# Kernel optimization log

Measured on AMD Instinct MI355X. Metric: run time of the kernel, lower is better.

## Reference

```python
import jax, jax.numpy as jnp
import numpy as np

B, T, V, D = 128, 128, 64, 32
Q, E, PLM = 5, 8, 768
D_STATIC, N_CLASS = 16, 2
ALPHA = 0.5


def _glorot(key, shape):
    lim = (6.0 / (shape[-2] + shape[-1])) ** 0.5
    return jax.random.uniform(key, shape, jnp.float32, -lim, lim)


def setup_inputs() -> dict:
    key = jax.random.key(0)
    ks = jax.random.split(key, 30)
    data = jax.random.normal(ks[0], (B, T, V), jnp.float32)
    mask = (jax.random.uniform(ks[1], (B, T, V)) < 0.3).astype(jnp.float32)
    P = jnp.concatenate([data, mask], axis=-1)  # [b, t, 2v]
    return {
        "P": P,
        "P_static": jax.random.normal(ks[2], (B, D_STATIC), jnp.float32),
        "P_avg_interval": jax.random.uniform(ks[3], (B, T, V)) * 10.0,
        "P_length": jax.random.randint(ks[4], (B, 1), T // 2, T + 1),
        "P_time": jax.random.uniform(ks[5], (B, T)),
        "P_var_plm_rep_tensor": jax.random.normal(ks[6], (V, PLM), jnp.float32),
        # Value_Encoder: Linear(1, D) + ReLU
        "w_val": _glorot(ks[7], (1, D))[0], "b_val": jnp.zeros((D,), jnp.float32),
        # Time_Encoder: periodic Linear(1, D-1), linear Linear(1, 1)
        "w_per": _glorot(ks[8], (1, D - 1))[0], "b_per": jnp.zeros((D - 1,), jnp.float32),
        "w_lin": _glorot(ks[9], (1, 1))[0], "b_lin": jnp.zeros((1,), jnp.float32),
        "emb1": jax.random.normal(ks[10], (V, D), jnp.float32),
        # prior_to_state MLP: PLM -> 2D -> Q
        "Ws1": _glorot(ks[11], (PLM, 2 * D)), "bs1": jnp.zeros((2 * D,), jnp.float32),
        "Ws2": _glorot(ks[12], (2 * D, Q)), "bs2": jnp.zeros((Q,), jnp.float32),
        # prior_to_graph MLP: PLM -> 2D -> E
        "Wg1": _glorot(ks[13], (PLM, 2 * D)), "bg1": jnp.zeros((2 * D,), jnp.float32),
        "Wg2": _glorot(ks[14], (2 * D, E)), "bg2": jnp.zeros((E,), jnp.float32),
        "rarity_W": jax.random.normal(ks[15], (V, V), jnp.float32),
        # hypernet gate params (nodes_num == Q): W [Q, 2D+1, D], b [Q, D]
        "Wu": _glorot(ks[16], (Q, 2 * D + 1, D)), "bu": _glorot(ks[17], (Q, D)),
        "Wr": _glorot(ks[18], (Q, 2 * D + 1, D)), "br": _glorot(ks[19], (Q, D)),
        "Wcand": _glorot(ks[20], (Q, 2 * D + 1, D)), "bcand": _glorot(ks[21], (Q, D)),
        # static embedding + classifier
        "W_se": _glorot(ks[22], (D_STATIC, V)), "b_se": jnp.zeros((V,), jnp.float32),
        "Wc1": _glorot(ks[23], (2 * V, 200)), "bc1": jnp.zeros((200,), jnp.float32),
        "Wc2": _glorot(ks[24], (200, N_CLASS)), "bc2": jnp.zeros((N_CLASS,), jnp.float32),
    }


def _forward(P, P_static, P_avg_interval, P_length, P_time, P_var_plm_rep_tensor,
             w_val, b_val, w_per, b_per, w_lin, b_lin, emb1,
             Ws1, bs1, Ws2, bs2, Wg1, bg1, Wg2, bg2, rarity_W,
             Wu, bu, Wr, br, Wcand, bcand, W_se, b_se, Wc1, bc1, Wc2, bc2):
    b, t, v2 = P.shape
    v = v2 // 2
    d = emb1.shape[1]
    data, mask = P[:, :, :v], P[:, :, v:]            # [b,t,v] each
    mk = mask[..., None]
    # embeddings: value + absolute time + node embedding, all masked
    value_emb = jax.nn.relu(data[..., None] * w_val + b_val) * mk          # [b,t,v,d]
    tt = P_time[:, :, None, None]                                          # [b,t,1,1]
    time_emb = jnp.concatenate([tt * w_lin + b_lin,
                                jnp.sin(tt * w_per + b_per)], -1) * mk     # [b,t,v,d]
    obs_emb = (value_emb + time_emb + emb1[None, None]) * mk               # [b,t,v,d]

    # PLM-prior hypernet vectors (identical across batch -> computed once, broadcast)
    var_vector = jax.nn.relu(P_var_plm_rep_tensor @ Ws1 + bs1) @ Ws2 + bs2  # [v,Q]
    gvec = jax.nn.relu(P_var_plm_rep_tensor @ Wg1 + bg1) @ Wg2 + bg2        # [v,E]
    gvec = gvec / jnp.maximum(jnp.linalg.norm(gvec, axis=-1, keepdims=True), 1e-12)
    adj = jax.nn.softmax(gvec @ gvec.T, axis=-1)                            # [v,v]

    var_total_obs = mask.sum(axis=1)                                        # [b,v]
    eye = jnp.eye(v, dtype=P.dtype)
    lengths = P_length[:, 0].astype(jnp.int32)                              # [b]

    def gate(inp, W, bb):
        # hypernet-generated per-node GRU gate: einsum('nd,dio->nio') + bmm, fused
        return (jnp.einsum('bvi,vq,qio->bvo', inp, var_vector, W)
                + jnp.einsum('vq,qo->vo', var_vector, bb))

    def step(carry, xs):
        h, out = carry
        cur_obs, m, cur_avg, s = xs
        rarity = ALPHA * jnp.tanh(cur_avg / (var_total_obs + 1.0))          # [b,v]
        rsm = -rarity_W * jnp.abs(rarity[:, :, None] - rarity[:, None, :])  # [b,v,v]
        amask = m[:, :, None] * m[:, None, :]   # rows of unobserved zeroed, observed cols = 1
        cur_adj = adj * (1.0 + rsm) * amask * (1.0 - eye) + eye             # [b,v,v]
        x = jnp.concatenate([cur_obs, rarity[..., None]], -1)               # [b,v,d+1]
        comb = jnp.einsum('bij,bjk->bik', cur_adj, jnp.concatenate([x, h], -1))
        r = jax.nn.sigmoid(gate(comb, Wr, br))
        u = jax.nn.sigmoid(gate(comb, Wu, bu))
        h_r = r * h  # original mutates h[nodes_ind] = r*h[nodes_ind] before candidate
        cand = jnp.tanh(gate(jnp.concatenate([x, h_r], -1), Wcand, bcand))
        h_new = (1.0 - u) * h_r + u * cand
        h = jnp.where((m > 0.5)[..., None], h_new, h)  # scatter only observed nodes
        out = jnp.where((s == lengths - 1)[:, None, None], h, out)
        return (h, out), None

    xs = (jnp.moveaxis(obs_emb, 1, 0), jnp.moveaxis(mask, 1, 0),
          jnp.moveaxis(P_avg_interval, 1, 0), jnp.arange(t, dtype=jnp.int32))
    h0 = jnp.zeros((b, v, d), P.dtype)
    (_, output), _ = jax.lax.scan(step, (h0, jnp.zeros_like(h0)), xs)

    static_emb = P_static @ W_se + b_se                                     # [b,v]
    feat = jnp.concatenate([output.sum(-1), static_emb], -1)                # [b,2v]
    return jax.nn.relu(feat @ Wc1 + bc1) @ Wc2 + bc2                        # [b,n_class]


def reference(P, P_static, P_avg_interval, P_length, P_time, P_var_plm_rep_tensor,
              w_val, b_val, w_per, b_per, w_lin, b_lin, emb1,
              Ws1, bs1, Ws2, bs2, Wg1, bg1, Wg2, bg2, rarity_W,
              Wu, bu, Wr, br, Wcand, bcand, W_se, b_se, Wc1, bc1, Wc2, bc2):
    return _forward(P, P_static, P_avg_interval, P_length, P_time, P_var_plm_rep_tensor,
                    w_val, b_val, w_per, b_per, w_lin, b_lin, emb1,
                    Ws1, bs1, Ws2, bs2, Wg1, bg1, Wg2, bg2, rarity_W,
                    Wu, bu, Wr, br, Wcand, bcand, W_se, b_se, Wc1, bc1, Wc2, bc2)
```

## Files before the change

kernel.cpp:

```cpp
#include <hip/hip_runtime.h>
#include <hip/hip_bf16.h>
#include <math.h>

#define BB 128
#define TT 128
#define VV 64
#define DD 32
#define NQ 5

typedef short bf16x8 __attribute__((ext_vector_type(8)));
typedef float f32x4 __attribute__((ext_vector_type(4)));

#define MFMA(a,b,c) __builtin_amdgcn_mfma_f32_16x16x32_bf16(a,b,c,0,0,0)
#define SB_DS() __builtin_amdgcn_sched_barrier(0x7F)

__device__ __forceinline__ float sigm(float x){ return 1.0f/(1.0f+__expf(-x)); }
__device__ __forceinline__ float tanhfast(float x){ return 2.0f/(1.0f+__expf(-2.0f*x)) - 1.0f; }
__device__ __forceinline__ unsigned short f2bf(float x){
  unsigned u = __float_as_uint(x);
  u += 0x7FFFu + ((u>>16)&1u);
  return (unsigned short)(u>>16);
}
__device__ __forceinline__ float bf2f(unsigned short h){
  return __uint_as_float(((unsigned)h)<<16);
}

union bfu { bf16x8 v; unsigned u[4]; unsigned short s[8]; };

__device__ __forceinline__ void split8(const float* x, bfu& H, bfu& L){
  #pragma unroll
  for (int i = 0; i < 4; ++i){
    const float a = x[2*i], c = x[2*i+1];
    const __hip_bfloat162 hp = __float22bfloat162_rn(make_float2(a, c));
    unsigned hu; __builtin_memcpy(&hu, &hp, 4);
    H.u[i] = hu;
    const float ah = __uint_as_float(hu << 16);
    const float ch = __uint_as_float(hu & 0xFFFF0000u);
    const __hip_bfloat162 lp = __float22bfloat162_rn(make_float2(a - ah, c - ch));
    unsigned lu; __builtin_memcpy(&lu, &lp, 4);
    L.u[i] = lu;
  }
}


__global__ __launch_bounds__(64)
void k_mlp(const float* __restrict__ Pplm,
           const float* __restrict__ Ws1, const float* __restrict__ bs1,
           const float* __restrict__ Ws2, const float* __restrict__ bs2,
           const float* __restrict__ Wg1, const float* __restrict__ bg1,
           const float* __restrict__ Wg2, const float* __restrict__ bg2,
           float* __restrict__ vv_ws, float* __restrict__ gn_ws)
{
  __shared__ float sH[64], sG[64], sgv[8];
  const int v = blockIdx.x, j = threadIdx.x;
  float a = bs1[j], g = bg1[j];
  for (int k = 0; k < 768; ++k){
    const float p = Pplm[v*768 + k];
    a = fmaf(p, Ws1[k*64 + j], a);
    g = fmaf(p, Wg1[k*64 + j], g);
  }
  sH[j] = fmaxf(a, 0.f);
  sG[j] = fmaxf(g, 0.f);
  __syncthreads();
  if (j < 5){
    float acc = bs2[j];
    for (int k = 0; k < 64; ++k) acc = fmaf(sH[k], Ws2[k*5 + j], acc);
    vv_ws[v*5 + j] = acc;
  }
  if (j < 8){
    float acc = bg2[j];
    for (int k = 0; k < 64; ++k) acc = fmaf(sG[k], Wg2[k*8 + j], acc);
    sgv[j] = acc;
  }
  __syncthreads();
  if (j == 0){
    float n = 0.f;
    for (int e = 0; e < 8; ++e) n += sgv[e]*sgv[e];
    n = fmaxf(sqrtf(n), 1e-12f);
    for (int e = 0; e < 8; ++e) gn_ws[v*8 + e] = sgv[e]/n;
  }
}

__global__ __launch_bounds__(64)
void k_adj(const float* __restrict__ gn_ws, float* __restrict__ adj_ws)
{
  const int v = blockIdx.x, j = threadIdx.x;
  float sc = 0.f;
  #pragma unroll
  for (int e = 0; e < 8; ++e) sc += gn_ws[v*8+e]*gn_ws[j*8+e];
  float mx = sc;
  for (int off = 32; off > 0; off >>= 1) mx = fmaxf(mx, __shfl_xor(mx, off));
  const float ex = __expf(sc - mx);
  float sm = ex;
  for (int off = 32; off > 0; off >>= 1) sm += __shfl_xor(sm, off);
  adj_ws[v*64 + j] = ex / sm;
}

__global__ __launch_bounds__(256)
void k_vto(const float* __restrict__ P, float* __restrict__ vto_ws)
{
  const int idx = blockIdx.x*256 + threadIdx.x;
  if (idx >= BB*VV) return;
  const int b = idx/VV, v = idx%VV;
  float s = 0.f;
  for (int t = 0; t < TT; ++t) s += P[((size_t)(b*TT+t))*128 + 64 + v];
  vto_ws[idx] = s;
}

__global__ __launch_bounds__(256)
void k_bpack(const float* __restrict__ Wr, const float* __restrict__ br,
             const float* __restrict__ Wu, const float* __restrict__ bu,
             const float* __restrict__ Wc, const float* __restrict__ bc,
             unsigned short* __restrict__ Bru, unsigned short* __restrict__ Bcn,
             float* __restrict__ sideRU, float* __restrict__ sideC)
{
  const int idx = blockIdx.x*256 + threadIdx.x;
  if (idx < 20480){
    const int f = idx >> 9, rem = idx & 511, l = rem >> 3, j = rem & 7;
    const int p = f & 1, kt = (f>>1)&1, e = f>>2;
    const int kp = kt*32 + (l>>4)*8 + j;
    const int k = (kp < 32) ? kp : kp + 1;
    const int o = p*16 + (l&15);
    const int q = (e < 5) ? e : e - 5;
    const float* W = (e < 5) ? Wr : Wu;
    Bru[idx] = f2bf(W[(q*65 + k)*32 + o]);
  } else if (idx < 30720){
    const int i2 = idx - 20480;
    const int f = i2 >> 9, rem = i2 & 511, l = rem >> 3, j = rem & 7;
    const int p = f & 1, kt = (f>>1)&1, e = f>>2;
    const int kp = kt*32 + (l>>4)*8 + j;
    const int k = (kp < 32) ? kp : kp + 1;
    const int o = p*16 + (l&15);
    Bcn[i2] = f2bf(Wc[(e*65 + k)*32 + o]);
  } else if (idx < 31360){
    const int i3 = idx - 30720;
    const int e = i3 >> 6, rem = i3 & 63, o = rem >> 1, s = rem & 1;
    const int q = (e < 5) ? e : e - 5;
    float v;
    if (s == 0) v = (e < 5) ? Wr[(q*65 + 32)*32 + o] : Wu[(q*65 + 32)*32 + o];
    else        v = (e < 5) ? br[q*32 + o] : bu[q*32 + o];
    sideRU[i3] = v;
  } else if (idx < 31680){
    const int i4 = idx - 31360;
    const int e = i4 >> 6, rem = i4 & 63, o = rem >> 1, s = rem & 1;
    sideC[i4] = s ? bc[e*32 + o] : Wc[(e*65 + 32)*32 + o];
  }
}


__global__ __launch_bounds__(256, 1)
void tedgn_main(const float* __restrict__ P, const float* __restrict__ Pstatic,
                const float* __restrict__ Pavg, const int* __restrict__ Plen,
                const float* __restrict__ Ptime,
                const float* __restrict__ w_val, const float* __restrict__ b_val,
                const float* __restrict__ w_per, const float* __restrict__ b_per,
                const float* __restrict__ w_lin, const float* __restrict__ b_lin,
                const float* __restrict__ emb1, const float* __restrict__ rarW,
                const float* __restrict__ Wse, const float* __restrict__ bse,
                const float* __restrict__ Wc1, const float* __restrict__ bc1,
                const float* __restrict__ Wc2, const float* __restrict__ bc2,
                const float* __restrict__ vv_ws, const float* __restrict__ adjb_ws,
                const float* __restrict__ vto_ws,
                const unsigned short* __restrict__ Bru_ws,
                const unsigned short* __restrict__ Bc_ws,
                const float* __restrict__ sideRU_ws, const float* __restrict__ sideC_ws,
                float* __restrict__ out)
{
  __shared__ __align__(16) unsigned short B0T[2][2][64][72];
  __shared__ __align__(16) unsigned short s_Wru[20480];
  __shared__ __align__(16) unsigned short s_Wc[10240];
  __shared__ __align__(16) float A1f[4][16][68];
  __shared__ __align__(16) float hrF[4][16][36];
  __shared__ __align__(16) float s_rar[2][64];
  __shared__ __align__(16) float s_m[2][64];
  __shared__ float s_sru[640], s_scd[320];
  __shared__ float s_outf[64][33];
  __shared__ float s_feat[128], s_hid[200];

  const int tid  = threadIdx.x;
  const int lane = tid & 63;
  const int wid  = tid >> 6;
  const int l15  = lane & 15;
  const int l16g = lane >> 4;
  const int kgo  = l16g * 8;
  const int R    = wid * 16;
  const int v_own = R + l15;
  const int b    = blockIdx.x;
  const int len  = Plen[b];

  for (int i = tid; i < 640; i += 256) s_sru[i] = sideRU_ws[i];
  for (int i = tid; i < 320; i += 256) s_scd[i] = sideC_ws[i];
  {
    const uint4* src1 = (const uint4*)Bru_ws;
    uint4* dst1 = (uint4*)s_Wru;
    for (int i = tid; i < 2560; i += 256) dst1[i] = src1[i];
    const uint4* src2 = (const uint4*)Bc_ws;
    uint4* dst2 = (uint4*)s_Wc;
    for (int i = tid; i < 1280; i += 256) dst2[i] = src2[i];
  }

  float adjb_r[2][8], rarW_r[2][8];
  #pragma unroll
  for (int kt = 0; kt < 2; ++kt)
    #pragma unroll
    for (int j = 0; j < 8; ++j){
      adjb_r[kt][j] = adjb_ws[v_own*64 + kt*32 + kgo + j];
      rarW_r[kt][j] = rarW   [v_own*64 + kt*32 + kgo + j];
    }
  float embr[8], wvr[8], bvr[8], wpr[8], bpr[8];
  #pragma unroll
  for (int j = 0; j < 8; ++j){
    const int d = kgo + j;
    embr[j] = emb1[v_own*DD + d];
    wvr[j]  = w_val[d];
    bvr[j]  = b_val[d];
    wpr[j]  = (d == 0) ? w_lin[0] : w_per[d-1];
    bpr[j]  = (d == 0) ? b_lin[0] : b_per[d-1];
  }
  float vvr[4][NQ];
  #pragma unroll
  for (int j = 0; j < 4; ++j)
    #pragma unroll
    for (int q = 0; q < NQ; ++q)
      vvr[j][q] = vv_ws[(R + l16g*4 + j)*NQ + q];
  const float vto_own = vto_ws[b*VV + v_own];

  float h[2][4]    = {{0.f,0.f,0.f,0.f},{0.f,0.f,0.f,0.f}};
  float outr[2][4] = {{0.f,0.f,0.f,0.f},{0.f,0.f,0.f,0.f}};
  bfu xfH, xfL;
  float rar_own, m_own;

  {
    const float pd = P[(size_t)(b*TT)*128 + v_own];
    const float pm = P[(size_t)(b*TT)*128 + 64 + v_own];
    const float pa = Pavg[(size_t)(b*TT)*VV + v_own];
    const float pt = Ptime[b*TT];
    const float rar_n = 0.5f * tanhfast(pa / (vto_own + 1.f));
    float xv[8];
    #pragma unroll
    for (int j = 0; j < 8; ++j){
      const int d = kgo + j;
      const float tearg = fmaf(pt, wpr[j], bpr[j]);
      const float te = (d == 0) ? tearg : __sinf(tearg);
      const float ve = fmaxf(fmaf(pd, wvr[j], bvr[j]), 0.f);
      xv[j] = (ve + te + embr[j]) * pm;
    }
    split8(xv, xfH, xfL);
    #pragma unroll
    for (int j = 0; j < 8; ++j){
      B0T[0][0][kgo + j][v_own] = xfH.s[j];
      B0T[0][1][kgo + j][v_own] = xfL.s[j];
    }
    *(uint2*)&B0T[0][0][32 + l15][R + l16g*4] = make_uint2(0u, 0u);
    *(uint2*)&B0T[0][1][32 + l15][R + l16g*4] = make_uint2(0u, 0u);
    *(uint2*)&B0T[0][0][48 + l15][R + l16g*4] = make_uint2(0u, 0u);
    *(uint2*)&B0T[0][1][48 + l15][R + l16g*4] = make_uint2(0u, 0u);
    if (l16g == 0){
      s_rar[0][v_own] = rar_n;
      s_m[0][v_own]   = pm;
    }
    rar_own = rar_n;
    m_own   = pm;
  }
  __syncthreads();

  #pragma clang loop unroll(disable)
  for (int t = 0; t < TT; ++t){
    const int cur = t & 1, nxt = cur ^ 1;

    float pd = 0.f, pm = 0.f, pa = 0.f, pt = 0.f;
    const bool more = (t + 1 < TT);
    if (more){
      pd = P[(size_t)(b*TT + t + 1)*128 + v_own];
      pm = P[(size_t)(b*TT + t + 1)*128 + 64 + v_own];
      pa = Pavg[(size_t)(b*TT + t + 1)*VV + v_own];
      pt = Ptime[b*TT + t + 1];
    }

    bfu aAh[2], aAl[2];
    float crar = 0.f;
    #pragma unroll
    for (int kt = 0; kt < 2; ++kt){
      const float4 r0 = *(const float4*)&s_rar[cur][kt*32 + kgo];
      const float4 r1 = *(const float4*)&s_rar[cur][kt*32 + kgo + 4];
      const float4 m0 = *(const float4*)&s_m[cur][kt*32 + kgo];
      const float4 m1 = *(const float4*)&s_m[cur][kt*32 + kgo + 4];
      const float rj[8] = {r0.x,r0.y,r0.z,r0.w,r1.x,r1.y,r1.z,r1.w};
      const float mj[8] = {m0.x,m0.y,m0.z,m0.w,m1.x,m1.y,m1.z,m1.w};
      float av[8];
      #pragma unroll
      for (int j = 0; j < 8; ++j){
        const int k = kt*32 + kgo + j;
        const float e1 = fmaf(-rarW_r[kt][j], fabsf(rar_own - rj[j]), 1.0f);
        const float a  = adjb_r[kt][j] * e1 * (m_own * mj[j]);
        av[j] = (k == v_own) ? 1.0f : a;
        crar = fmaf(av[j], rj[j], crar);
      }
      split8(av, aAh[kt], aAl[kt]);
    }
    crar += __shfl_xor(crar, 16);
    crar += __shfl_xor(crar, 32);
    if (l16g == 0) A1f[wid][l15][64] = crar;

    #pragma unroll
    for (int n = 0; n < 4; ++n){
      f32x4 acc = {0.f,0.f,0.f,0.f};
      #pragma unroll
      for (int kt = 0; kt < 2; ++kt){
        const bf16x8 bh = *(const bf16x8*)&B0T[cur][0][n*16 + l15][kt*32 + kgo];
        const bf16x8 bl = *(const bf16x8*)&B0T[cur][1][n*16 + l15][kt*32 + kgo];
        acc = MFMA(aAh[kt].v, bh, acc);
        acc = MFMA(aAl[kt].v, bh, acc);
        acc = MFMA(aAh[kt].v, bl, acc);
      }
      const int col = n*16 + l15;
      #pragma unroll
      for (int j = 0; j < 4; ++j) A1f[wid][l16g*4 + j][col] = acc[j];
    }
    SB_DS();

    bfu aH[2], aL[2];
    #pragma unroll
    for (int kt = 0; kt < 2; ++kt){
      float xv[8];
      *(float4*)&xv[0] = *(const float4*)&A1f[wid][l15][kt*32 + kgo];
      *(float4*)&xv[4] = *(const float4*)&A1f[wid][l15][kt*32 + kgo + 4];
      split8(xv, aH[kt], aL[kt]);
    }
    float a64f[4];
    #pragma unroll
    for (int j = 0; j < 4; ++j) a64f[j] = A1f[wid][l16g*4 + j][64];

    float hr[2][4], uu[2][4];
    {
      f32x4 ag[10][2];
      #pragma unroll
      for (int e = 0; e < 10; ++e)
        #pragma unroll
        for (int p2 = 0; p2 < 2; ++p2){
          const float2 wb = *(const float2*)&s_sru[e*64 + (p2*16 + l15)*2];
          #pragma unroll
          for (int j = 0; j < 4; ++j) ag[e][p2][j] = fmaf(a64f[j], wb.x, wb.y);
        }
      #pragma unroll
      for (int e = 0; e < 10; ++e)
        #pragma unroll
        for (int p2 = 0; p2 < 2; ++p2){
          const bf16x8 w0 = *(const bf16x8*)&s_Wru[(((e*2+0)*2+p2)*64 + lane)*8];
          const bf16x8 w1 = *(const bf16x8*)&s_Wru[(((e*2+1)*2+p2)*64 + lane)*8];
          ag[e][p2] = MFMA(aH[0].v, w0, ag[e][p2]);
          ag[e][p2] = MFMA(aL[0].v, w0, ag[e][p2]);
          ag[e][p2] = MFMA(aH[1].v, w1, ag[e][p2]);
          ag[e][p2] = MFMA(aL[1].v, w1, ag[e][p2]);
        }
      #pragma unroll
      for (int p2 = 0; p2 < 2; ++p2)
        #pragma unroll
        for (int j = 0; j < 4; ++j){
          const float pr = vvr[j][0]*ag[0][p2][j] + vvr[j][1]*ag[1][p2][j]
                         + vvr[j][2]*ag[2][p2][j] + vvr[j][3]*ag[3][p2][j]
                         + vvr[j][4]*ag[4][p2][j];
          hr[p2][j] = sigm(pr) * h[p2][j];
          hrF[wid][l16g*4 + j][p2*16 + l15] = hr[p2][j];
        }
      #pragma unroll
      for (int p2 = 0; p2 < 2; ++p2)
        #pragma unroll
        for (int j = 0; j < 4; ++j){
          const float pu = vvr[j][0]*ag[5][p2][j] + vvr[j][1]*ag[6][p2][j]
                         + vvr[j][2]*ag[7][p2][j] + vvr[j][3]*ag[8][p2][j]
                         + vvr[j][4]*ag[9][p2][j];
          uu[p2][j] = sigm(pu);
        }
    }
    SB_DS();

    {
      bfu hH, hL;
      {
        float hv[8];
        *(float4*)&hv[0] = *(const float4*)&hrF[wid][l15][kgo];
        *(float4*)&hv[4] = *(const float4*)&hrF[wid][l15][kgo + 4];
        split8(hv, hH, hL);
      }
      float rar_cj[4], m_cj[4];
      #pragma unroll
      for (int j = 0; j < 4; ++j){
        rar_cj[j] = s_rar[cur][R + l16g*4 + j];
        m_cj[j]   = s_m[cur][R + l16g*4 + j];
      }
      f32x4 ag[5][2];
      #pragma unroll
      for (int e = 0; e < 5; ++e)
        #pragma unroll
        for (int p2 = 0; p2 < 2; ++p2){
          const float2 wb = *(const float2*)&s_scd[e*64 + (p2*16 + l15)*2];
          #pragma unroll
          for (int j = 0; j < 4; ++j) ag[e][p2][j] = fmaf(rar_cj[j], wb.x, wb.y);
        }
      #pragma unroll
      for (int e = 0; e < 5; ++e)
        #pragma unroll
        for (int p2 = 0; p2 < 2; ++p2){
          const bf16x8 w0 = *(const bf16x8*)&s_Wc[(((e*2+0)*2+p2)*64 + lane)*8];
          const bf16x8 w1 = *(const bf16x8*)&s_Wc[(((e*2+1)*2+p2)*64 + lane)*8];
          ag[e][p2] = MFMA(xfH.v, w0, ag[e][p2]);
          ag[e][p2] = MFMA(xfL.v, w0, ag[e][p2]);
          ag[e][p2] = MFMA(hH.v,  w1, ag[e][p2]);
          ag[e][p2] = MFMA(hL.v,  w1, ag[e][p2]);
        }
      const bool snap = (t == len - 1);
      #pragma unroll
      for (int p2 = 0; p2 < 2; ++p2)
        #pragma unroll
        for (int j = 0; j < 4; ++j){
          const float pc = vvr[j][0]*ag[0][p2][j] + vvr[j][1]*ag[1][p2][j]
                         + vvr[j][2]*ag[2][p2][j] + vvr[j][3]*ag[3][p2][j]
                         + vvr[j][4]*ag[4][p2][j];
          const float cd = tanhfast(pc);
          const float hn = fmaf(uu[p2][j], cd - hr[p2][j], hr[p2][j]);
          const float hf = (m_cj[j] > 0.5f) ? hn : h[p2][j];
          h[p2][j] = hf;
          if (snap) outr[p2][j] = hf;
        }
    }

    {
      float h8[8] = {h[0][0],h[0][1],h[0][2],h[0][3],h[1][0],h[1][1],h[1][2],h[1][3]};
      bfu HH, HL;
      split8(h8, HH, HL);
      *(uint2*)&B0T[nxt][0][32 + l15][R + l16g*4] = make_uint2(HH.u[0], HH.u[1]);
      *(uint2*)&B0T[nxt][1][32 + l15][R + l16g*4] = make_uint2(HL.u[0], HL.u[1]);
      *(uint2*)&B0T[nxt][0][48 + l15][R + l16g*4] = make_uint2(HH.u[2], HH.u[3]);
      *(uint2*)&B0T[nxt][1][48 + l15][R + l16g*4] = make_uint2(HL.u[2], HL.u[3]);
    }

    if (more){
      const float rar_n = 0.5f * tanhfast(pa / (vto_own + 1.f));
      float xv[8];
      #pragma unroll
      for (int j = 0; j < 8; ++j){
        const int d = kgo + j;
        const float tearg = fmaf(pt, wpr[j], bpr[j]);
        const float te = (d == 0) ? tearg : __sinf(tearg);
        const float ve = fmaxf(fmaf(pd, wvr[j], bvr[j]), 0.f);
        xv[j] = (ve + te + embr[j]) * pm;
      }
      split8(xv, xfH, xfL);
      #pragma unroll
      for (int j = 0; j < 8; ++j){
        B0T[nxt][0][kgo + j][v_own] = xfH.s[j];
        B0T[nxt][1][kgo + j][v_own] = xfL.s[j];
      }
      if (l16g == 0){
        s_rar[nxt][v_own] = rar_n;
        s_m[nxt][v_own]   = pm;
      }
      rar_own = rar_n;
      m_own   = pm;
    }
    __syncthreads();
  }

  #pragma unroll
  for (int p2 = 0; p2 < 2; ++p2)
    #pragma unroll
    for (int j = 0; j < 4; ++j)
      s_outf[R + l16g*4 + j][p2*16 + l15] = outr[p2][j];
  __syncthreads();
  if (tid < VV){
    float s = 0.f;
    #pragma unroll
    for (int d = 0; d < DD; ++d) s += s_outf[tid][d];
    s_feat[tid] = s;
  } else if (tid < 2*VV){
    const int v = tid - VV;
    float se = bse[v];
    #pragma unroll
    for (int k = 0; k < 16; ++k) se = fmaf(Pstatic[b*16 + k], Wse[k*VV + v], se);
    s_feat[VV + v] = se;
  }
  __syncthreads();
  if (tid < 200){
    float a = bc1[tid];
    for (int k = 0; k < 128; ++k) a = fmaf(s_feat[k], Wc1[k*200 + tid], a);
    s_hid[tid] = fmaxf(a, 0.f);
  }
  __syncthreads();
  if (tid < 2){
    float a = bc2[tid];
    for (int k = 0; k < 200; ++k) a = fmaf(s_hid[k], Wc2[k*2 + tid], a);
    out[b*2 + tid] = a;
  }
}


extern "C" void kernel_launch(void* const* d_in, const int* in_sizes, int n_in,
                              void* d_out, int out_size, void* d_ws, size_t ws_size,
                              hipStream_t stream) {
  (void)in_sizes; (void)n_in; (void)out_size; (void)ws_size;
  const float* P       = (const float*)d_in[0];
  const float* Pstatic = (const float*)d_in[1];
  const float* Pavg    = (const float*)d_in[2];
  const int*   Plen    = (const int*)  d_in[3];
  const float* Ptime   = (const float*)d_in[4];
  const float* Pplm    = (const float*)d_in[5];
  const float* w_val   = (const float*)d_in[6];
  const float* b_val   = (const float*)d_in[7];
  const float* w_per   = (const float*)d_in[8];
  const float* b_per   = (const float*)d_in[9];
  const float* w_lin   = (const float*)d_in[10];
  const float* b_lin   = (const float*)d_in[11];
  const float* emb1    = (const float*)d_in[12];
  const float* Ws1     = (const float*)d_in[13];
  const float* bs1     = (const float*)d_in[14];
  const float* Ws2     = (const float*)d_in[15];
  const float* bs2     = (const float*)d_in[16];
  const float* Wg1     = (const float*)d_in[17];
  const float* bg1     = (const float*)d_in[18];
  const float* Wg2     = (const float*)d_in[19];
  const float* bg2     = (const float*)d_in[20];
  const float* rarW    = (const float*)d_in[21];
  const float* Wu      = (const float*)d_in[22];
  const float* bu      = (const float*)d_in[23];
  const float* Wr      = (const float*)d_in[24];
  const float* br      = (const float*)d_in[25];
  const float* Wcand   = (const float*)d_in[26];
  const float* bcand   = (const float*)d_in[27];
  const float* Wse     = (const float*)d_in[28];
  const float* bse     = (const float*)d_in[29];
  const float* Wc1     = (const float*)d_in[30];
  const float* bc1     = (const float*)d_in[31];
  const float* Wc2     = (const float*)d_in[32];
  const float* bc2     = (const float*)d_in[33];

  float* ws = (float*)d_ws;
  float*          vv_ws   = ws;
  float*          gn_ws   = ws + 320;
  float*          adjb_ws = ws + 832;
  float*          vto_ws  = ws + 4928;
  unsigned short* Bru_ws  = (unsigned short*)(ws + 13120);
  unsigned short* Bc_ws   = (unsigned short*)(ws + 23360);
  float*          sideRU_ws = ws + 28480;
  float*          sideC_ws  = ws + 29120;

  k_mlp  <<<64, 64, 0, stream>>>(Pplm, Ws1, bs1, Ws2, bs2, Wg1, bg1, Wg2, bg2, vv_ws, gn_ws);
  k_adj  <<<64, 64, 0, stream>>>(gn_ws, adjb_ws);
  k_vto  <<<(BB*VV + 255)/256, 256, 0, stream>>>(P, vto_ws);
  k_bpack<<<124, 256, 0, stream>>>(Wr, br, Wu, bu, Wcand, bcand, Bru_ws, Bc_ws, sideRU_ws, sideC_ws);

  tedgn_main<<<BB, 256, 0, stream>>>(P, Pstatic, Pavg, Plen, Ptime,
                                     w_val, b_val, w_per, b_per, w_lin, b_lin,
                                     emb1, rarW, Wse, bse, Wc1, bc1, Wc2, bc2,
                                     vv_ws, adjb_ws, vto_ws,
                                     Bru_ws, Bc_ws, sideRU_ws, sideC_ws,
                                     (float*)d_out);
}
```

Measured before the change: 623.4 us.

## Split each row-block across two waves by output half, doubling block to 512 threads

The main recurrent kernel now launches 512 threads per batch element. Each pair of waves shares a 16-row block and splits the 32 hidden output columns between them, so each wave does half the MFMA work for the gate and candidate products. The aim is to shorten the serial per-timestep critical path by spreading the work over more waves per CU. In exchange it replaces the wave-local sched barriers with two extra block-wide __syncthreads per timestep, and the adjacency/rarity computation is duplicated in both waves of each pair.

```diff
diff --git a/kernel.cpp b/kernel.cpp
--- a/kernel.cpp
+++ b/kernel.cpp
@@ -12,7 +12,6 @@
 typedef float f32x4 __attribute__((ext_vector_type(4)));
 
 #define MFMA(a,b,c) __builtin_amdgcn_mfma_f32_16x16x32_bf16(a,b,c,0,0,0)
-#define SB_DS() __builtin_amdgcn_sched_barrier(0x7F)
 
 __device__ __forceinline__ float sigm(float x){ return 1.0f/(1.0f+__expf(-x)); }
 __device__ __forceinline__ float tanhfast(float x){ return 2.0f/(1.0f+__expf(-2.0f*x)) - 1.0f; }
@@ -39,6 +38,21 @@
     const __hip_bfloat162 lp = __float22bfloat162_rn(make_float2(a - ah, c - ch));
     unsigned lu; __builtin_memcpy(&lu, &lp, 4);
     L.u[i] = lu;
+  }
+}
+
+__device__ __forceinline__ void split4(const float* x, unsigned* H, unsigned* L){
+  #pragma unroll
+  for (int i = 0; i < 2; ++i){
+    const float a = x[2*i], c = x[2*i+1];
+    const __hip_bfloat162 hp = __float22bfloat162_rn(make_float2(a, c));
+    unsigned hu; __builtin_memcpy(&hu, &hp, 4);
+    H[i] = hu;
+    const float ah = __uint_as_float(hu << 16);
+    const float ch = __uint_as_float(hu & 0xFFFF0000u);
+    const __hip_bfloat162 lp = __float22bfloat162_rn(make_float2(a - ah, c - ch));
+    unsigned lu; __builtin_memcpy(&lu, &lp, 4);
+    L[i] = lu;
   }
 }
 
@@ -148,7 +162,7 @@
 }
 
 
-__global__ __launch_bounds__(256, 1)
+__global__ __launch_bounds__(512, 1)
 void tedgn_main(const float* __restrict__ P, const float* __restrict__ Pstatic,
                 const float* __restrict__ Pavg, const int* __restrict__ Plen,
                 const float* __restrict__ Ptime,
@@ -180,23 +194,26 @@
   const int tid  = threadIdx.x;
   const int lane = tid & 63;
   const int wid  = tid >> 6;
+  const int mq   = wid >> 1;
+  const int ph   = wid & 1;
   const int l15  = lane & 15;
   const int l16g = lane >> 4;
   const int kgo  = l16g * 8;
-  const int R    = wid * 16;
+  const int R    = mq * 16;
   const int v_own = R + l15;
+  const int oo   = ph*16 + l15;
   const int b    = blockIdx.x;
   const int len  = Plen[b];
 
-  for (int i = tid; i < 640; i += 256) s_sru[i] = sideRU_ws[i];
-  for (int i = tid; i < 320; i += 256) s_scd[i] = sideC_ws[i];
+  for (int i = tid; i < 640; i += 512) s_sru[i] = sideRU_ws[i];
+  for (int i = tid; i < 320; i += 512) s_scd[i] = sideC_ws[i];
   {
     const uint4* src1 = (const uint4*)Bru_ws;
     uint4* dst1 = (uint4*)s_Wru;
-    for (int i = tid; i < 2560; i += 256) dst1[i] = src1[i];
+    for (int i = tid; i < 2560; i += 512) dst1[i] = src1[i];
     const uint4* src2 = (const uint4*)Bc_ws;
     uint4* dst2 = (uint4*)s_Wc;
-    for (int i = tid; i < 1280; i += 256) dst2[i] = src2[i];
+    for (int i = tid; i < 1280; i += 512) dst2[i] = src2[i];
   }
 
   float adjb_r[2][8], rarW_r[2][8];
@@ -225,8 +242,8 @@
       vvr[j][q] = vv_ws[(R + l16g*4 + j)*NQ + q];
   const float vto_own = vto_ws[b*VV + v_own];
 
-  float h[2][4]    = {{0.f,0.f,0.f,0.f},{0.f,0.f,0.f,0.f}};
-  float outr[2][4] = {{0.f,0.f,0.f,0.f},{0.f,0.f,0.f,0.f}};
+  float h[4]    = {0.f,0.f,0.f,0.f};
+  float outr[4] = {0.f,0.f,0.f,0.f};
   bfu xfH, xfL;
   float rar_own, m_own;
 
@@ -246,18 +263,21 @@
       xv[j] = (ve + te + embr[j]) * pm;
     }
     split8(xv, xfH, xfL);
-    #pragma unroll
-    for (int j = 0; j < 8; ++j){
-      B0T[0][0][kgo + j][v_own] = xfH.s[j];
-      B0T[0][1][kgo + j][v_own] = xfL.s[j];
-    }
-    *(uint2*)&B0T[0][0][32 + l15][R + l16g*4] = make_uint2(0u, 0u);
-    *(uint2*)&B0T[0][1][32 + l15][R + l16g*4] = make_uint2(0u, 0u);
-    *(uint2*)&B0T[0][0][48 + l15][R + l16g*4] = make_uint2(0u, 0u);
-    *(uint2*)&B0T[0][1][48 + l15][R + l16g*4] = make_uint2(0u, 0u);
-    if (l16g == 0){
-      s_rar[0][v_own] = rar_n;
-      s_m[0][v_own]   = pm;
+    if (ph == 0){
+      #pragma unroll
+      for (int j = 0; j < 8; ++j){
+        B0T[0][0][kgo + j][v_own] = xfH.s[j];
+        B0T[0][1][kgo + j][v_own] = xfL.s[j];
+      }
+      *(uint2*)&B0T[0][0][32 + l15][R + l16g*4] = make_uint2(0u, 0u);
+      *(uint2*)&B0T[0][1][32 + l15][R + l16g*4] = make_uint2(0u, 0u);
+      if (l16g == 0){
+        s_rar[0][v_own] = rar_n;
+        s_m[0][v_own]   = pm;
+      }
+    } else {
+      *(uint2*)&B0T[0][0][48 + l15][R + l16g*4] = make_uint2(0u, 0u);
+      *(uint2*)&B0T[0][1][48 + l15][R + l16g*4] = make_uint2(0u, 0u);
     }
     rar_own = rar_n;
     m_own   = pm;
@@ -277,110 +297,105 @@
       pt = Ptime[b*TT + t + 1];
     }
 
-    bfu aAh[2], aAl[2];
-    float crar = 0.f;
-    #pragma unroll
-    for (int kt = 0; kt < 2; ++kt){
-      const float4 r0 = *(const float4*)&s_rar[cur][kt*32 + kgo];
-      const float4 r1 = *(const float4*)&s_rar[cur][kt*32 + kgo + 4];
-      const float4 m0 = *(const float4*)&s_m[cur][kt*32 + kgo];
-      const float4 m1 = *(const float4*)&s_m[cur][kt*32 + kgo + 4];
-      const float rj[8] = {r0.x,r0.y,r0.z,r0.w,r1.x,r1.y,r1.z,r1.w};
-      const float mj[8] = {m0.x,m0.y,m0.z,m0.w,m1.x,m1.y,m1.z,m1.w};
-      float av[8];
-      #pragma unroll
-      for (int j = 0; j < 8; ++j){
-        const int k = kt*32 + kgo + j;
-        const float e1 = fmaf(-rarW_r[kt][j], fabsf(rar_own - rj[j]), 1.0f);
-        const float a  = adjb_r[kt][j] * e1 * (m_own * mj[j]);
-        av[j] = (k == v_own) ? 1.0f : a;
-        crar = fmaf(av[j], rj[j], crar);
-      }
-      split8(av, aAh[kt], aAl[kt]);
-    }
-    crar += __shfl_xor(crar, 16);
-    crar += __shfl_xor(crar, 32);
-    if (l16g == 0) A1f[wid][l15][64] = crar;
-
-    #pragma unroll
-    for (int n = 0; n < 4; ++n){
-      f32x4 acc = {0.f,0.f,0.f,0.f};
+    {
+      bfu aAh[2], aAl[2];
+      float crar = 0.f;
       #pragma unroll
       for (int kt = 0; kt < 2; ++kt){
-        const bf16x8 bh = *(const bf16x8*)&B0T[cur][0][n*16 + l15][kt*32 + kgo];
-        const bf16x8 bl = *(const bf16x8*)&B0T[cur][1][n*16 + l15][kt*32 + kgo];
-        acc = MFMA(aAh[kt].v, bh, acc);
-        acc = MFMA(aAl[kt].v, bh, acc);
-        acc = MFMA(aAh[kt].v, bl, acc);
-      }
-      const int col = n*16 + l15;
-      #pragma unroll
-      for (int j = 0; j < 4; ++j) A1f[wid][l16g*4 + j][col] = acc[j];
-    }
-    SB_DS();
-
-    bfu aH[2], aL[2];
-    #pragma unroll
-    for (int kt = 0; kt < 2; ++kt){
-      float xv[8];
-      *(float4*)&xv[0] = *(const float4*)&A1f[wid][l15][kt*32 + kgo];
-      *(float4*)&xv[4] = *(const float4*)&A1f[wid][l15][kt*32 + kgo + 4];
-      split8(xv, aH[kt], aL[kt]);
-    }
-    float a64f[4];
-    #pragma unroll
-    for (int j = 0; j < 4; ++j) a64f[j] = A1f[wid][l16g*4 + j][64];
-
-    float hr[2][4], uu[2][4];
+        const float4 r0 = *(const float4*)&s_rar[cur][kt*32 + kgo];
+        const float4 r1 = *(const float4*)&s_rar[cur][kt*32 + kgo + 4];
+        const float4 m0 = *(const float4*)&s_m[cur][kt*32 + kgo];
+        const float4 m1 = *(const float4*)&s_m[cur][kt*32 + kgo + 4];
+        const float rj[8] = {r0.x,r0.y,r0.z,r0.w,r1.x,r1.y,r1.z,r1.w};
+        const float mj[8] = {m0.x,m0.y,m0.z,m0.w,m1.x,m1.y,m1.z,m1.w};
+        float av[8];
+        #pragma unroll
+        for (int j = 0; j < 8; ++j){
+          const int k = kt*32 + kgo + j;
+          const float e1 = fmaf(-rarW_r[kt][j], fabsf(rar_own - rj[j]), 1.0f);
+          const float a  = adjb_r[kt][j] * e1 * (m_own * mj[j]);
+          av[j] = (k == v_own) ? 1.0f : a;
+          crar = fmaf(av[j], rj[j], crar);
+        }
+        split8(av, aAh[kt], aAl[kt]);
+      }
+      crar += __shfl_xor(crar, 16);
+      crar += __shfl_xor(crar, 32);
+      if (ph == 0 && l16g == 0) A1f[mq][l15][64] = crar;
+
+      #pragma unroll
+      for (int ni = 0; ni < 2; ++ni){
+        const int n = 2*ph + ni;
+        f32x4 acc = {0.f,0.f,0.f,0.f};
+        #pragma unroll
+        for (int kt = 0; kt < 2; ++kt){
+          const bf16x8 bh = *(const bf16x8*)&B0T[cur][0][n*16 + l15][kt*32 + kgo];
+          const bf16x8 bl = *(const bf16x8*)&B0T[cur][1][n*16 + l15][kt*32 + kgo];
+          acc = MFMA(aAh[kt].v, bh, acc);
+          acc = MFMA(aAl[kt].v, bh, acc);
+          acc = MFMA(aAh[kt].v, bl, acc);
+        }
+        const int col = n*16 + l15;
+        #pragma unroll
+        for (int j = 0; j < 4; ++j) A1f[mq][l16g*4 + j][col] = acc[j];
+      }
+    }
+    __syncthreads();
+
+    float hr[4], uu[4];
     {
-      f32x4 ag[10][2];
-      #pragma unroll
-      for (int e = 0; e < 10; ++e)
+      bfu aH[2], aL[2];
+      #pragma unroll
+      for (int kt = 0; kt < 2; ++kt){
+        float xv[8];
+        *(float4*)&xv[0] = *(const float4*)&A1f[mq][l15][kt*32 + kgo];
+        *(float4*)&xv[4] = *(const float4*)&A1f[mq][l15][kt*32 + kgo + 4];
+        split8(xv, aH[kt], aL[kt]);
+      }
+      float a64f[4];
+      #pragma unroll
+      for (int j = 0; j < 4; ++j) a64f[j] = A1f[mq][l16g*4 + j][64];
+
+      f32x4 ag[10];
+      #pragma unroll
+      for (int e = 0; e < 10; ++e){
+        const float2 wb = *(const float2*)&s_sru[e*64 + oo*2];
         #pragma unroll
-        for (int p2 = 0; p2 < 2; ++p2){
-          const float2 wb = *(const float2*)&s_sru[e*64 + (p2*16 + l15)*2];
-          #pragma unroll
-          for (int j = 0; j < 4; ++j) ag[e][p2][j] = fmaf(a64f[j], wb.x, wb.y);
-        }
-      #pragma unroll
-      for (int e = 0; e < 10; ++e)
-        #pragma unroll
-        for (int p2 = 0; p2 < 2; ++p2){
-          const bf16x8 w0 = *(const bf16x8*)&s_Wru[(((e*2+0)*2+p2)*64 + lane)*8];
-          const bf16x8 w1 = *(const bf16x8*)&s_Wru[(((e*2+1)*2+p2)*64 + lane)*8];
-          ag[e][p2] = MFMA(aH[0].v, w0, ag[e][p2]);
-          ag[e][p2] = MFMA(aL[0].v, w0, ag[e][p2]);
-          ag[e][p2] = MFMA(aH[1].v, w1, ag[e][p2]);
-          ag[e][p2] = MFMA(aL[1].v, w1, ag[e][p2]);
-        }
-      #pragma unroll
-      for (int p2 = 0; p2 < 2; ++p2)
-        #pragma unroll
-        for (int j = 0; j < 4; ++j){
-          const float pr = vvr[j][0]*ag[0][p2][j] + vvr[j][1]*ag[1][p2][j]
-                         + vvr[j][2]*ag[2][p2][j] + vvr[j][3]*ag[3][p2][j]
-                         + vvr[j][4]*ag[4][p2][j];
-          hr[p2][j] = sigm(pr) * h[p2][j];
-          hrF[wid][l16g*4 + j][p2*16 + l15] = hr[p2][j];
-        }
-      #pragma unroll
-      for (int p2 = 0; p2 < 2; ++p2)
-        #pragma unroll
-        for (int j = 0; j < 4; ++j){
-          const float pu = vvr[j][0]*ag[5][p2][j] + vvr[j][1]*ag[6][p2][j]
-                         + vvr[j][2]*ag[7][p2][j] + vvr[j][3]*ag[8][p2][j]
-                         + vvr[j][4]*ag[9][p2][j];
-          uu[p2][j] = sigm(pu);
-        }
-    }
-    SB_DS();
+        for (int j = 0; j < 4; ++j) ag[e][j] = fmaf(a64f[j], wb.x, wb.y);
+      }
+      #pragma unroll
+      for (int e = 0; e < 10; ++e){
+        const bf16x8 w0 = *(const bf16x8*)&s_Wru[(((e*2+0)*2+ph)*64 + lane)*8];
+        const bf16x8 w1 = *(const bf16x8*)&s_Wru[(((e*2+1)*2+ph)*64 + lane)*8];
+        ag[e] = MFMA(aH[0].v, w0, ag[e]);
+        ag[e] = MFMA(aL[0].v, w0, ag[e]);
+        ag[e] = MFMA(aH[1].v, w1, ag[e]);
+        ag[e] = MFMA(aL[1].v, w1, ag[e]);
+      }
+      #pragma unroll
+      for (int j = 0; j < 4; ++j){
+        const float pr = vvr[j][0]*ag[0][j] + vvr[j][1]*ag[1][j]
+                       + vvr[j][2]*ag[2][j] + vvr[j][3]*ag[3][j]
+                       + vvr[j][4]*ag[4][j];
+        hr[j] = sigm(pr) * h[j];
+        hrF[mq][l16g*4 + j][oo] = hr[j];
+      }
+      #pragma unroll
+      for (int j = 0; j < 4; ++j){
+        const float pu = vvr[j][0]*ag[5][j] + vvr[j][1]*ag[6][j]
+                       + vvr[j][2]*ag[7][j] + vvr[j][3]*ag[8][j]
+                       + vvr[j][4]*ag[9][j];
+        uu[j] = sigm(pu);
+      }
+    }
+    __syncthreads();
 
     {
       bfu hH, hL;
       {
         float hv[8];
-        *(float4*)&hv[0] = *(const float4*)&hrF[wid][l15][kgo];
-        *(float4*)&hv[4] = *(const float4*)&hrF[wid][l15][kgo + 4];
+        *(float4*)&hv[0] = *(const float4*)&hrF[mq][l15][kgo];
+        *(float4*)&hv[4] = *(const float4*)&hrF[mq][l15][kgo + 4];
         split8(hv, hH, hL);
       }
       float rar_cj[4], m_cj[4];
@@ -389,84 +404,73 @@
         rar_cj[j] = s_rar[cur][R + l16g*4 + j];
         m_cj[j]   = s_m[cur][R + l16g*4 + j];
       }
-      f32x4 ag[5][2];
-      #pragma unroll
-      for (int e = 0; e < 5; ++e)
+      f32x4 ag[5];
+      #pragma unroll
+      for (int e = 0; e < 5; ++e){
+        const float2 wb = *(const float2*)&s_scd[e*64 + oo*2];
         #pragma unroll
-        for (int p2 = 0; p2 < 2; ++p2){
-          const float2 wb = *(const float2*)&s_scd[e*64 + (p2*16 + l15)*2];
+        for (int j = 0; j < 4; ++j) ag[e][j] = fmaf(rar_cj[j], wb.x, wb.y);
+      }
+      #pragma unroll
+      for (int e = 0; e < 5; ++e){
+        const bf16x8 w0 = *(const bf16x8*)&s_Wc[(((e*2+0)*2+ph)*64 + lane)*8];
+        const bf16x8 w1 = *(const bf16x8*)&s_Wc[(((e*2+1)*2+ph)*64 + lane)*8];
+        ag[e] = MFMA(xfH.v, w0, ag[e]);
+        ag[e] = MFMA(xfL.v, w0, ag[e]);
+        ag[e] = MFMA(hH.v,  w1, ag[e]);
+        ag[e] = MFMA(hL.v,  w1, ag[e]);
+      }
+      const bool snap = (t == len - 1);
+      #pragma unroll
+      for (int j = 0; j < 4; ++j){
+        const float pc = vvr[j][0]*ag[0][j] + vvr[j][1]*ag[1][j]
+                       + vvr[j][2]*ag[2][j] + vvr[j][3]*ag[3][j]
+                       + vvr[j][4]*ag[4][j];
+        const float cd = tanhfast(pc);
+        const float hn = fmaf(uu[j], cd - hr[j], hr[j]);
+        const float hf = (m_cj[j] > 0.5f) ? hn : h[j];
+        h[j] = hf;
+        if (snap) outr[j] = hf;
+      }
+      {
+        unsigned H2[2], L2[2];
+        split4(h, H2, L2);
+        *(uint2*)&B0T[nxt][0][32 + oo][R + l16g*4] = make_uint2(H2[0], H2[1]);
+        *(uint2*)&B0T[nxt][1][32 + oo][R + l16g*4] = make_uint2(L2[0], L2[1]);
+      }
+      if (more){
+        const float rar_n = 0.5f * tanhfast(pa / (vto_own + 1.f));
+        float xv[8];
+        #pragma unroll
+        for (int j = 0; j < 8; ++j){
+          const int d = kgo + j;
+          const float tearg = fmaf(pt, wpr[j], bpr[j]);
+          const float te = (d == 0) ? tearg : __sinf(tearg);
+          const float ve = fmaxf(fmaf(pd, wvr[j], bvr[j]), 0.f);
+          xv[j] = (ve + te + embr[j]) * pm;
+        }
+        split8(xv, xfH, xfL);
+        if (ph == 0){
           #pragma unroll
-          for (int j = 0; j < 4; ++j) ag[e][p2][j] = fmaf(rar_cj[j], wb.x, wb.y);
+          for (int j = 0; j < 8; ++j){
+            B0T[nxt][0][kgo + j][v_own] = xfH.s[j];
+            B0T[nxt][1][kgo + j][v_own] = xfL.s[j];
+          }
+          if (l16g == 0){
+            s_rar[nxt][v_own] = rar_n;
+            s_m[nxt][v_own]   = pm;
+          }
         }
-      #pragma unroll
-      for (int e = 0; e < 5; ++e)
-        #pragma unroll
-        for (int p2 = 0; p2 < 2; ++p2){
-          const bf16x8 w0 = *(const bf16x8*)&s_Wc[(((e*2+0)*2+p2)*64 + lane)*8];
-          const bf16x8 w1 = *(const bf16x8*)&s_Wc[(((e*2+1)*2+p2)*64 + lane)*8];
-          ag[e][p2] = MFMA(xfH.v, w0, ag[e][p2]);
-          ag[e][p2] = MFMA(xfL.v, w0, ag[e][p2]);
-          ag[e][p2] = MFMA(hH.v,  w1, ag[e][p2]);
-          ag[e][p2] = MFMA(hL.v,  w1, ag[e][p2]);
-        }
-      const bool snap = (t == len - 1);
-      #pragma unroll
-      for (int p2 = 0; p2 < 2; ++p2)
-        #pragma unroll
-        for (int j = 0; j < 4; ++j){
-          const float pc = vvr[j][0]*ag[0][p2][j] + vvr[j][1]*ag[1][p2][j]
-                         + vvr[j][2]*ag[2][p2][j] + vvr[j][3]*ag[3][p2][j]
-                         + vvr[j][4]*ag[4][p2][j];
-          const float cd = tanhfast(pc);
-          const float hn = fmaf(uu[p2][j], cd - hr[p2][j], hr[p2][j]);
-          const float hf = (m_cj[j] > 0.5f) ? hn : h[p2][j];
-          h[p2][j] = hf;
-          if (snap) outr[p2][j] = hf;
-        }
-    }
-
-    {
-      float h8[8] = {h[0][0],h[0][1],h[0][2],h[0][3],h[1][0],h[1][1],h[1][2],h[1][3]};
-      bfu HH, HL;
-      split8(h8, HH, HL);
-      *(uint2*)&B0T[nxt][0][32 + l15][R + l16g*4] = make_uint2(HH.u[0], HH.u[1]);
-      *(uint2*)&B0T[nxt][1][32 + l15][R + l16g*4] = make_uint2(HL.u[0], HL.u[1]);
-      *(uint2*)&B0T[nxt][0][48 + l15][R + l16g*4] = make_uint2(HH.u[2], HH.u[3]);
-      *(uint2*)&B0T[nxt][1][48 + l15][R + l16g*4] = make_uint2(HL.u[2], HL.u[3]);
-    }
-
-    if (more){
-      const float rar_n = 0.5f * tanhfast(pa / (vto_own + 1.f));
-      float xv[8];
-      #pragma unroll
-      for (int j = 0; j < 8; ++j){
-        const int d = kgo + j;
-        const float tearg = fmaf(pt, wpr[j], bpr[j]);
-        const float te = (d == 0) ? tearg : __sinf(tearg);
-        const float ve = fmaxf(fmaf(pd, wvr[j], bvr[j]), 0.f);
-        xv[j] = (ve + te + embr[j]) * pm;
-      }
-      split8(xv, xfH, xfL);
-      #pragma unroll
-      for (int j = 0; j < 8; ++j){
-        B0T[nxt][0][kgo + j][v_own] = xfH.s[j];
-        B0T[nxt][1][kgo + j][v_own] = xfL.s[j];
-      }
-      if (l16g == 0){
-        s_rar[nxt][v_own] = rar_n;
-        s_m[nxt][v_own]   = pm;
-      }
-      rar_own = rar_n;
-      m_own   = pm;
+        rar_own = rar_n;
+        m_own   = pm;
+      }
     }
     __syncthreads();
   }
 
   #pragma unroll
-  for (int p2 = 0; p2 < 2; ++p2)
-    #pragma unroll
-    for (int j = 0; j < 4; ++j)
-      s_outf[R + l16g*4 + j][p2*16 + l15] = outr[p2][j];
+  for (int j = 0; j < 4; ++j)
+    s_outf[R + l16g*4 + j][oo] = outr[j];
   __syncthreads();
   if (tid < VV){
     float s = 0.f;
@@ -549,7 +553,7 @@
   k_vto  <<<(BB*VV + 255)/256, 256, 0, stream>>>(P, vto_ws);
   k_bpack<<<124, 256, 0, stream>>>(Wr, br, Wu, bu, Wcand, bcand, Bru_ws, Bc_ws, sideRU_ws, sideC_ws);
 
-  tedgn_main<<<BB, 256, 0, stream>>>(P, Pstatic, Pavg, Plen, Ptime,
+  tedgn_main<<<BB, 512, 0, stream>>>(P, Pstatic, Pavg, Plen, Ptime,
                                      w_val, b_val, w_per, b_per, w_lin, b_lin,
                                      emb1, rarW, Wse, bse, Wc1, bc1, Wc2, bc2,
                                      vv_ws, adjb_ws, vto_ws,
```

Result: faster. 586.2 us (-6.0%).
